# Kernel optimization log

Hardware: AMD Instinct MI355X
Metric: run time of the kernel (lower is better)

Reference implementation:

```python
import jax, jax.numpy as jnp
from jax import lax
import numpy as np


def setup_inputs() -> dict:
    key = jax.random.key(0)
    T, W = 2048, 30  # document length, max span width
    starts = jnp.repeat(jnp.arange(T, dtype=jnp.int32), W)      # [T*W]
    widths = jnp.tile(jnp.arange(W, dtype=jnp.int32), T)        # [T*W]
    ends = jnp.minimum(starts + widths, T - 1)
    spans = jnp.stack([starts, ends], axis=1)                   # [N,2], N=61440
    N = spans.shape[0]
    scores = jax.random.normal(key, (N,), dtype=jnp.float32)
    mask = jnp.ones((N,), dtype=jnp.float32)
    return {
        "spans": spans,
        "span_mention_scores": scores,
        "span_mask": mask,
        "token_num": T,
        "num_spans_to_keep": int(0.4 * T),
    }


def _greedy_non_crossing(spans, scores, mask, T, k):
    """Greedy NMS-style selection of up to k spans with no crossing overlap.
    Faithful to masked_topk_non_overlap: iterate candidates in descending
    (score + log(mask)) order; a candidate (s,e) is rejected iff it crosses
    an already-selected span, tracked via start_to_max_end / end_to_min_start
    tables. Sequential dependence expressed as lax.scan; the O(span_width)
    inner token loop is vectorized as an O(T) masked range query.
    """
    N = scores.shape[0]
    order = jnp.argsort(-(scores + jnp.log(mask)))  # descending sort
    starts = spans[:, 0].astype(jnp.int32)
    ends = spans[:, 1].astype(jnp.int32)
    tok = jnp.arange(T, dtype=jnp.int32)

    def step(carry, c):
        s2e, e2s, sel, cnt = carry
        s = starts[c]
        e = ends[c]
        # token_idx in (s, e] with start_to_max_end[token_idx] > e -> crossing
        cross1 = jnp.any((tok > s) & (tok <= e) & (s2e > e))
        # token_idx in [s, e) with 0 <= end_to_min_start[token_idx] < s -> crossing
        cross2 = jnp.any((tok >= s) & (tok < e) & (e2s >= 0) & (e2s < s))
        accept = jnp.logical_and(jnp.logical_not(cross1 | cross2), cnt < k)
        # start_to_max_end[s] = max(old, e) if accepted
        s2e = s2e.at[s].set(jnp.where(accept, jnp.maximum(s2e[s], e), s2e[s]))
        # end_to_min_start[e] = s if unset or s smaller, if accepted
        cur = e2s[e]
        e2s = e2s.at[e].set(jnp.where(accept & ((cur == -1) | (s < cur)), s, cur))
        sel = sel.at[c].set(sel[c] | accept)
        cnt = cnt + accept.astype(jnp.int32)
        return (s2e, e2s, sel, cnt), None

    init = (jnp.full((T,), -1, dtype=jnp.int32),
            jnp.full((T,), -1, dtype=jnp.int32),
            jnp.zeros((N,), dtype=bool),
            jnp.int32(0))
    (s2e, e2s, sel, cnt), _ = lax.scan(step, init, order)

    # sort selected candidates by (start, end); pad to fixed size k
    sort_key = jnp.where(sel, starts * T + ends, T * T)  # T*T > any valid key
    idx = jnp.argsort(sort_key)[:k]
    valid = jnp.arange(k) < cnt
    top_idx = jnp.where(valid, idx, 0)
    return top_idx, valid


def reference(spans, span_mention_scores, span_mask, token_num, num_spans_to_keep):
    top_idx, valid = _greedy_non_crossing(
        spans, span_mention_scores, span_mask, token_num, num_spans_to_keep)
    top_scores = jnp.where(valid, span_mention_scores[top_idx], 0.0)
    top_spans = jnp.where(valid[:, None], spans[top_idx], 0)
    return top_scores, top_idx, top_spans, valid
```

## Files before the change

kernel.cpp:

```cpp
#include <hip/hip_runtime.h>
#include <math.h>
#include <limits.h>

#define TPB   1024
#define TILE  1024
#define MAXT  2048
#define TPAD  64
#define MAXK  1024
#define MAXW  29
#define BATCH 1024
#define FLAGSTRIDE 16

struct SortSM {
  union {
    unsigned h[4 * 256];
    unsigned wcnt[16][256];
  };
  unsigned baseL[256];
  unsigned part[4][256];
};

__device__ inline void dbar(unsigned* flg, int nblk) {
  __syncthreads();
  if (threadIdx.x == 0) {
    __threadfence();
    atomicExch(&flg[blockIdx.x * FLAGSTRIDE], 1u);
  }
  if ((int)threadIdx.x < nblk) {
    int spin = 0;
    while (__hip_atomic_load(&flg[threadIdx.x * FLAGSTRIDE], __ATOMIC_ACQUIRE,
                             __HIP_MEMORY_SCOPE_AGENT) == 0u) {
      __builtin_amdgcn_s_sleep(2);
      if ((++spin & 255) == 0) {
        if (atomicAdd(&flg[threadIdx.x * FLAGSTRIDE], 0u) != 0u) break;
      }
    }
  }
  __syncthreads();
  if (threadIdx.x == 0) __threadfence();
  __syncthreads();
}

__global__ void __launch_bounds__(TPB, 4) sort_kernel(
    const float* __restrict__ scores, const float* __restrict__ mask,
    int N, int nT, unsigned* pflag, unsigned* ghist,
    unsigned* tileCnt, unsigned* keysA, unsigned* keysB, int* idxA, int* idxB) {
  __shared__ SortSM s;
  __shared__ unsigned base4[4][256];
  const int tid = threadIdx.x;
  const int lane = tid & 63;
  const int wave = tid >> 6;

  if (tid < 1024) s.h[tid] = 0;
  __syncthreads();
  {
    int i = blockIdx.x * TILE + tid;
    if (i < N) {
      float kf = scores[i] + logf(mask[i]);
      unsigned u = __float_as_uint(kf);
      u = (u & 0x80000000u) ? ~u : (u | 0x80000000u);
      u = ~u;
      keysA[i] = u;
      atomicAdd(&s.h[(u & 255u)], 1u);
      atomicAdd(&s.h[256 + ((u >> 8) & 255u)], 1u);
      atomicAdd(&s.h[512 + ((u >> 16) & 255u)], 1u);
      atomicAdd(&s.h[768 + (u >> 24)], 1u);
    }
    __syncthreads();
    if (tid < 1024 && s.h[tid]) atomicAdd(&ghist[tid], s.h[tid]);
  }
  dbar(pflag + (size_t)4 * nT * FLAGSTRIDE, nT);

  if (wave < 4) {
    const int p = wave;
    unsigned v0 = ghist[p * 256 + 4 * lane + 0];
    unsigned v1 = ghist[p * 256 + 4 * lane + 1];
    unsigned v2 = ghist[p * 256 + 4 * lane + 2];
    unsigned v3 = ghist[p * 256 + 4 * lane + 3];
    unsigned sum = v0 + v1 + v2 + v3;
    unsigned x = sum;
    for (int off = 1; off < 64; off <<= 1) {
      unsigned y = __shfl_up(x, off, 64);
      if (lane >= off) x += y;
    }
    unsigned excl = x - sum;
    base4[p][4 * lane + 0] = excl;
    base4[p][4 * lane + 1] = excl + v0;
    base4[p][4 * lane + 2] = excl + v0 + v1;
    base4[p][4 * lane + 3] = excl + v0 + v1 + v2;
  }
  __syncthreads();

  for (int p = 0; p < 4; ++p) {
    const unsigned* srck = (p & 1) ? keysB : keysA;
    const int*      srci = (p & 1) ? idxB : idxA;
    unsigned*       dstk = (p & 1) ? keysA : keysB;
    int*            dsti = (p & 1) ? idxA : idxB;
    const int shift = 8 * p;
    unsigned* flg = pflag + (size_t)p * nT * FLAGSTRIDE;

    for (int j = tid; j < 16 * 256; j += TPB)
      (&s.wcnt[0][0])[j] = 0;
    __syncthreads();

    int i = blockIdx.x * TILE + tid;
    bool v = (i < N);
    unsigned key = v ? srck[i] : 0u;
    int pay = v ? ((p == 0) ? i : srci[i]) : 0;
    unsigned d = (key >> shift) & 255u;
    unsigned long long mm = __ballot(v);
    #pragma unroll
    for (int b = 0; b < 8; ++b) {
      unsigned long long bb = __ballot((d >> b) & 1u);
      mm &= ((d >> b) & 1u) ? bb : ~bb;
    }
    unsigned rnk = (unsigned)__popcll(mm & ((1ull << lane) - 1ull));
    if (v && rnk == 0) s.wcnt[wave][d] = (unsigned)__popcll(mm);
    __syncthreads();
    if (tid < 256) {
      unsigned run = 0;
      #pragma unroll
      for (int g = 0; g < 16; ++g) {
        unsigned c = s.wcnt[g][tid];
        s.wcnt[g][tid] = run;
        run += c;
      }
      tileCnt[blockIdx.x * 256 + tid] = run;
    }
    __syncthreads();

    if (tid == 0) {
      __threadfence();
      atomicExch(&flg[blockIdx.x * FLAGSTRIDE], 1u);
    }
    if (tid < blockIdx.x) {
      while (atomicAdd(&flg[tid * FLAGSTRIDE], 0u) == 0u)
        __builtin_amdgcn_s_sleep(2);
    }
    __syncthreads();
    if (tid == 0) __threadfence();
    __syncthreads();

    {
      int digit = tid & 255;
      int chunk = tid >> 8;
      int b = blockIdx.x;
      int Q = (b + 3) >> 2;
      int t0 = chunk * Q;
      int t1 = t0 + Q; if (t1 > b) t1 = b;
      unsigned acc2 = 0;
      for (int t = t0; t < t1; ++t)
        acc2 += tileCnt[t * 256 + digit];
      s.part[chunk][digit] = acc2;
    }
    __syncthreads();
    if (tid < 256) {
      s.baseL[tid] = base4[p][tid] + s.part[0][tid] + s.part[1][tid]
                   + s.part[2][tid] + s.part[3][tid];
    }
    __syncthreads();
    if (v) {
      unsigned pos = s.baseL[d] + s.wcnt[wave][d] + rnk;
      dstk[pos] = key;
      dsti[pos] = pay;
    }
    if (p < 3) dbar(pflag + (size_t)(5 + p) * nT * FLAGSTRIDE, nT);
  }
}

__device__ inline bool precheck30(const unsigned* tabP, int cc, int cs, int ce) {
  if (cc < 0) return false;
  int w = ce - cs;
  bool crossed = false;
  #pragma unroll
  for (int off = 0; off <= MAXW; ++off) {
    unsigned tv = tabP[cs + off];
    crossed |= ((off >= 1) & (off <= w) & ((tv & 0xFFFFu) > (unsigned)(ce + 1)))
             | ((off < w) & ((tv >> 16) < (unsigned)cs));
  }
  for (int off = MAXW + 1; off <= w; ++off) {
    unsigned tv = tabP[cs + off];
    crossed |= ((tv & 0xFFFFu) > (unsigned)(ce + 1));
    if (off < w) crossed |= ((tv >> 16) < (unsigned)cs);
  }
  return !crossed;
}

__global__ void __launch_bounds__(TPB, 4) greedy_kernel(
    const int2* __restrict__ spans2, const int* __restrict__ spans,
    const float* __restrict__ scores, const int* __restrict__ order,
    const int* __restrict__ tnum_p, const int* __restrict__ keep_p,
    float* __restrict__ out, int N) {
  __shared__ unsigned tabP[MAXT + TPAD];
  __shared__ int2 tab[MAXT + TPAD];
  __shared__ unsigned long long acc[MAXK];
  __shared__ unsigned long long surv[BATCH];
  __shared__ unsigned long long Cmat[BATCH];
  __shared__ int wvs[16];
  __shared__ int gcnt;

  const int tid = threadIdx.x;
  const int lane = tid & 63;
  const int wave = tid >> 6;
  const int T  = tnum_p[0];
  const int k0 = keep_p[0];
  const int k  = (k0 < MAXK) ? k0 : MAXK;

  for (int t = tid; t < MAXT + TPAD; t += TPB) {
    tab[t] = make_int2(-1, INT_MAX);
    tabP[t] = 0xFFFF0000u;
  }
  if (tid == 0) gcnt = 0;
  __syncthreads();

  int cc = -1, cs = 0, ce = 0, nn = -1;
  if (tid < N)         cc = order[tid];
  if (BATCH + tid < N) nn = order[BATCH + tid];
  if (cc >= 0) { int2 sp = spans2[cc]; cs = sp.x; ce = sp.y; }

  int cnt = 0;
  for (int c0 = 0; c0 < N && cnt < k; c0 += BATCH) {
    int pc = nn, ps = 0, pe = 0;
    if (pc >= 0) { int2 sp = spans2[pc]; ps = sp.x; pe = sp.y; }
    int i2 = c0 + 2 * BATCH + tid;
    nn = (i2 < N) ? order[i2] : -1;

    bool ok = precheck30(tabP, cc, cs, ce);
    unsigned long long bal = __ballot(ok);
    if (lane == 0) wvs[wave] = (int)__popcll(bal);
    __syncthreads();
    int ns = 0, wb = 0;
    #pragma unroll
    for (int w2 = 0; w2 < 16; ++w2) {
      if (w2 == wave) wb = ns;
      ns += wvs[w2];
    }

    if (ns > 0) {
      if (ok) {
        int pos = wb + (int)__popcll(bal & ((1ull << lane) - 1ull));
        surv[pos] = ((unsigned long long)(unsigned)cs << 48)
                  | ((unsigned long long)(unsigned)ce << 32)
                  | (unsigned)cc;
      }
      __syncthreads();

      for (int v = tid; v < ns; v += TPB) {
        unsigned long long pk = surv[v];
        int gs = (int)(pk >> 48), ge = (int)((pk >> 32) & 0xFFFFu);
        int gbase = v & ~63;
        int m = ns - gbase; if (m > 64) m = 64;
        unsigned long long C = 0;
        for (int j = 0; j < m; ++j) {
          unsigned long long pj = surv[gbase + j];
          int sj = (int)(pj >> 48), ej = (int)((pj >> 32) & 0xFFFFu);
          bool cr = (gs < sj && sj <= ge && ej > ge) ||
                    (sj < gs && gs <= ej && ej < ge);
          C |= (unsigned long long)cr << j;
        }
        Cmat[v] = C;
      }
      __syncthreads();

      if (tid < 64) {
        bool dirty = false;
        for (int g = 0; g < ns && cnt < k; g += 64) {
          int m = ns - g; if (m > 64) m = 64;
          bool act = lane < m;
          int gs = 0, ge = 0, gc = 0;
          unsigned long long C = 0;
          if (act) {
            unsigned long long pk = surv[g + lane];
            gs = (int)(pk >> 48);
            ge = (int)((pk >> 32) & 0xFFFFu);
            gc = (int)(unsigned)pk;
            C  = Cmat[g + lane];
          }
          bool pre = act;
          if (dirty) {
            pre = act && precheck30(tabP, gc, gs, ge);
          }
          unsigned long long preB = __ballot(pre);
          if (preB == 0ull) continue;
          int np = (int)__popcll(preB);
          unsigned long long lower = (1ull << lane) - 1ull;
          unsigned long long accm;
          int cnt0g = cnt;
          if (np == 1) {
            accm = preB;
            cnt += 1;
          } else {
            unsigned long long Cl = C & lower;
            unsigned long long resolvedB = ~preB;
            accm = 0ull;
            while (true) {
              bool meUn   = ((resolvedB >> lane) & 1ull) == 0ull;
              bool killed = (Cl & accm) != 0ull;
              bool ready  = (Cl & ~resolvedB) == 0ull;
              unsigned long long newacc = __ballot(meUn && ready && !killed);
              unsigned long long newrej = __ballot(meUn && killed);
              if (!(newacc | newrej)) break;
              accm |= newacc;
              resolvedB |= (newacc | newrej);
            }
            int nacc = (int)__popcll(accm);
            if (cnt + nacc > k) {
              int room = k - cnt;
              bool a0 = ((accm >> lane) & 1ull) != 0ull;
              int ar = (int)__popcll(accm & lower);
              accm = __ballot(a0 && (ar < room));
              nacc = room;
            }
            cnt += nacc;
          }
          bool accme = ((accm >> lane) & 1ull) != 0ull;
          if (accme) {
            int rank = (int)__popcll(accm & lower);
            acc[cnt0g + rank] =
                ((unsigned long long)(unsigned)(gs * T + ge) << 32) | (unsigned)gc;
            atomicMax(&tab[gs].x, ge);
            atomicMin(&tab[ge].y, gs);
          }
          if (accme) {
            int2 tv = tab[gs];
            tabP[gs] = ((unsigned)(tv.y > 65535 ? 65535 : tv.y) << 16)
                     | (unsigned)(tv.x + 1);
            int2 tv2 = tab[ge];
            tabP[ge] = ((unsigned)(tv2.y > 65535 ? 65535 : tv2.y) << 16)
                     | (unsigned)(tv2.x + 1);
          }
          if (accm) dirty = true;
        }
        if (lane == 0) gcnt = cnt;
      }
      __syncthreads();
      cnt = gcnt;
    }

    cc = pc; cs = ps; ce = pe;
  }

  int M = 2;
  while (M < cnt) M <<= 1;
  for (int j = tid; j < M; j += TPB)
    if (j >= cnt) acc[j] = ~0ull;
  __syncthreads();
  for (int kk = 2; kk <= M; kk <<= 1) {
    for (int jj = kk >> 1; jj > 0; jj >>= 1) {
      for (int i3 = tid; i3 < M; i3 += TPB) {
        int ixj = i3 ^ jj;
        if (ixj > i3) {
          unsigned long long a = acc[i3], b = acc[ixj];
          bool up = ((i3 & kk) == 0);
          if ((a > b) == up) { acc[i3] = b; acc[ixj] = a; }
        }
      }
      __syncthreads();
    }
  }

  for (int j = tid; j < k0; j += TPB) {
    if (j < cnt) {
      int cand = (int)(acc[j] & 0xFFFFFFFFu);
      out[j]                  = scores[cand];
      out[k0 + j]             = (float)cand;
      out[2 * k0 + 2 * j]     = (float)spans[2 * cand];
      out[2 * k0 + 2 * j + 1] = (float)spans[2 * cand + 1];
      out[4 * k0 + j]         = 1.0f;
    } else {
      out[j]                  = 0.0f;
      out[k0 + j]             = 0.0f;
      out[2 * k0 + 2 * j]     = 0.0f;
      out[2 * k0 + 2 * j + 1] = 0.0f;
      out[4 * k0 + j]         = 0.0f;
    }
  }
}

extern "C" void kernel_launch(void* const* d_in, const int* in_sizes, int n_in,
                              void* d_out, int out_size, void* d_ws, size_t ws_size,
                              hipStream_t stream) {
  const int*   spans  = (const int*)d_in[0];
  const float* scores = (const float*)d_in[1];
  const float* mask   = (const float*)d_in[2];
  const int*   tnum   = (const int*)d_in[3];
  const int*   keep   = (const int*)d_in[4];
  const int N = in_sizes[1];
  const int nT = (N + TILE - 1) / TILE;

  unsigned* pflag   = (unsigned*)d_ws;
  unsigned* ghist   = pflag + (size_t)8 * nT * FLAGSTRIDE;
  unsigned* tileCnt = ghist + 1024;
  unsigned* keysA   = tileCnt + (size_t)nT * 256;
  unsigned* keysB   = keysA + N;
  int*      idxA    = (int*)(keysB + N);
  int*      idxB    = idxA + N;
  float*    out     = (float*)d_out;

  hipMemsetAsync(pflag, 0,
                 ((size_t)8 * nT * FLAGSTRIDE + 1024) * sizeof(unsigned),
                 stream);

  sort_kernel<<<nT, TPB, 0, stream>>>(scores, mask, N, nT, pflag, ghist,
                                      tileCnt, keysA, keysB, idxA, idxB);
  greedy_kernel<<<1, TPB, 0, stream>>>((const int2*)spans, spans, scores,
                                       idxA, tnum, keep, out, N);
}
```

Measured before the change: 227.6 us.

## Warp-specialize greedy loop: wave 0 resolves while other waves prefilter next batch

Splits the block into a resolver wave and 15 producer waves. The producers precheck candidates and build the crossing matrix for the next batch into double-buffered shared arrays, while wave 0 runs the sequential greedy acceptance on the previous batch. Producers coordinate through a spin-based LDS barrier, and the batch size drops to 960 to match the 15 producer waves. This aims to hide the serial resolve phase behind the parallel filter, but producers now precheck against a table that is one batch stale, so wave 0 must always rerun the precheck, and every iteration adds spin-wait overhead.

Result: faster. 219.6 us, median of 2 (-3.5%).

```diff
diff --git a/kernel.cpp b/kernel.cpp
--- a/kernel.cpp
+++ b/kernel.cpp
@@ -8,7 +8,7 @@
 #define TPAD  64
 #define MAXK  1024
 #define MAXW  29
-#define BATCH 1024
+#define BATCH 960
 #define FLAGSTRIDE 16
 
 struct SortSM {
@@ -186,6 +186,15 @@
   return !crossed;
 }
 
+__device__ inline void softbar(unsigned* sbar, unsigned target) {
+  if ((threadIdx.x & 63) == 0)
+    __hip_atomic_fetch_add(sbar, 1u, __ATOMIC_ACQ_REL,
+                           __HIP_MEMORY_SCOPE_WORKGROUP);
+  while (__hip_atomic_load(sbar, __ATOMIC_ACQUIRE,
+                           __HIP_MEMORY_SCOPE_WORKGROUP) < target)
+    __builtin_amdgcn_s_sleep(1);
+}
+
 __global__ void __launch_bounds__(TPB, 4) greedy_kernel(
     const int2* __restrict__ spans2, const int* __restrict__ spans,
     const float* __restrict__ scores, const int* __restrict__ order,
@@ -194,9 +203,11 @@
   __shared__ unsigned tabP[MAXT + TPAD];
   __shared__ int2 tab[MAXT + TPAD];
   __shared__ unsigned long long acc[MAXK];
-  __shared__ unsigned long long surv[BATCH];
-  __shared__ unsigned long long Cmat[BATCH];
+  __shared__ unsigned long long surv0[BATCH], surv1[BATCH];
+  __shared__ unsigned long long cmat0[BATCH], cmat1[BATCH];
   __shared__ int wvs[16];
+  __shared__ int ns_s[2];
+  __shared__ unsigned sbar;
   __shared__ int gcnt;
 
   const int tid = threadIdx.x;
@@ -210,134 +221,137 @@
     tab[t] = make_int2(-1, INT_MAX);
     tabP[t] = 0xFFFF0000u;
   }
-  if (tid == 0) gcnt = 0;
+  if (tid == 0) { gcnt = 0; ns_s[0] = 0; ns_s[1] = 0; sbar = 0u; }
+  if (tid < 16) wvs[tid] = 0;
   __syncthreads();
 
   int cc = -1, cs = 0, ce = 0, nn = -1;
-  if (tid < N)         cc = order[tid];
-  if (BATCH + tid < N) nn = order[BATCH + tid];
-  if (cc >= 0) { int2 sp = spans2[cc]; cs = sp.x; ce = sp.y; }
-
+  if (tid >= 64) {
+    int q = tid - 64;
+    if (q < N)          cc = order[q];
+    if (BATCH + q < N)  nn = order[BATCH + q];
+    if (cc >= 0) { int2 sp = spans2[cc]; cs = sp.x; ce = sp.y; }
+  }
+
+  unsigned long long* sA = surv0; unsigned long long* cA = cmat0;
+  unsigned long long* sB = surv1; unsigned long long* cB = cmat1;
+  int bufA = 0;
   int cnt = 0;
-  for (int c0 = 0; c0 < N && cnt < k; c0 += BATCH) {
-    int pc = nn, ps = 0, pe = 0;
-    if (pc >= 0) { int2 sp = spans2[pc]; ps = sp.x; pe = sp.y; }
-    int i2 = c0 + 2 * BATCH + tid;
-    nn = (i2 < N) ? order[i2] : -1;
-
-    bool ok = precheck30(tabP, cc, cs, ce);
-    unsigned long long bal = __ballot(ok);
-    if (lane == 0) wvs[wave] = (int)__popcll(bal);
-    __syncthreads();
-    int ns = 0, wb = 0;
-    #pragma unroll
-    for (int w2 = 0; w2 < 16; ++w2) {
-      if (w2 == wave) wb = ns;
-      ns += wvs[w2];
-    }
-
-    if (ns > 0) {
+  int it = 0;
+  for (long c0 = 0; c0 < (long)N + BATCH && cnt < k; c0 += BATCH, ++it) {
+    if (wave == 0) {
+      int nsA = ns_s[bufA];
+      for (int g = 0; g < nsA && cnt < k; g += 64) {
+        int m = nsA - g; if (m > 64) m = 64;
+        bool act = lane < m;
+        int gs = 0, ge = 0, gc = 0;
+        unsigned long long C = 0;
+        if (act) {
+          unsigned long long pk = sA[g + lane];
+          gs = (int)(pk >> 48);
+          ge = (int)((pk >> 32) & 0xFFFFu);
+          gc = (int)(unsigned)pk;
+          C  = cA[g + lane];
+        }
+        bool pre = act && precheck30(tabP, gc, gs, ge);
+        unsigned long long preB = __ballot(pre);
+        if (preB == 0ull) continue;
+        int np = (int)__popcll(preB);
+        unsigned long long lower = (1ull << lane) - 1ull;
+        unsigned long long accm;
+        int cnt0g = cnt;
+        if (np == 1) {
+          accm = preB;
+          cnt += 1;
+        } else {
+          unsigned long long Cl = C & lower;
+          unsigned long long resolvedB = ~preB;
+          accm = 0ull;
+          while (true) {
+            bool meUn   = ((resolvedB >> lane) & 1ull) == 0ull;
+            bool killed = (Cl & accm) != 0ull;
+            bool ready  = (Cl & ~resolvedB) == 0ull;
+            unsigned long long newacc = __ballot(meUn && ready && !killed);
+            unsigned long long newrej = __ballot(meUn && killed);
+            if (!(newacc | newrej)) break;
+            accm |= newacc;
+            resolvedB |= (newacc | newrej);
+          }
+          int nacc = (int)__popcll(accm);
+          if (cnt + nacc > k) {
+            int room = k - cnt;
+            bool a0 = ((accm >> lane) & 1ull) != 0ull;
+            int ar = (int)__popcll(accm & lower);
+            accm = __ballot(a0 && (ar < room));
+            nacc = room;
+          }
+          cnt += nacc;
+        }
+        bool accme = ((accm >> lane) & 1ull) != 0ull;
+        if (accme) {
+          int rank = (int)__popcll(accm & lower);
+          acc[cnt0g + rank] =
+              ((unsigned long long)(unsigned)(gs * T + ge) << 32) | (unsigned)gc;
+          atomicMax(&tab[gs].x, ge);
+          atomicMin(&tab[ge].y, gs);
+        }
+        if (accme) {
+          int2 tv = tab[gs];
+          tabP[gs] = ((unsigned)(tv.y > 65535 ? 65535 : tv.y) << 16)
+                   | (unsigned)(tv.x + 1);
+          int2 tv2 = tab[ge];
+          tabP[ge] = ((unsigned)(tv2.y > 65535 ? 65535 : tv2.y) << 16)
+                   | (unsigned)(tv2.x + 1);
+        }
+      }
+      if (lane == 0) gcnt = cnt;
+    } else {
+      int q = tid - 64;
+      int pc = nn, ps = 0, pe = 0;
+      if (pc >= 0) { int2 sp = spans2[pc]; ps = sp.x; pe = sp.y; }
+      long i2 = c0 + 2 * (long)BATCH + q;
+      nn = (i2 < N) ? order[i2] : -1;
+
+      bool ok = precheck30(tabP, cc, cs, ce);
+      unsigned long long bal = __ballot(ok);
+      if (lane == 0) wvs[wave] = (int)__popcll(bal);
+      softbar(&sbar, 15u * (2u * (unsigned)it + 1u));
+      int ns = 0, wb = 0;
+      #pragma unroll
+      for (int w2 = 1; w2 < 16; ++w2) {
+        if (w2 == wave) wb = ns;
+        ns += wvs[w2];
+      }
       if (ok) {
         int pos = wb + (int)__popcll(bal & ((1ull << lane) - 1ull));
-        surv[pos] = ((unsigned long long)(unsigned)cs << 48)
-                  | ((unsigned long long)(unsigned)ce << 32)
-                  | (unsigned)cc;
-      }
-      __syncthreads();
-
-      for (int v = tid; v < ns; v += TPB) {
-        unsigned long long pk = surv[v];
+        sB[pos] = ((unsigned long long)(unsigned)cs << 48)
+                | ((unsigned long long)(unsigned)ce << 32)
+                | (unsigned)cc;
+      }
+      if (wave == 1 && lane == 0) ns_s[bufA ^ 1] = ns;
+      softbar(&sbar, 15u * (2u * (unsigned)it + 2u));
+      for (int v = q; v < ns; v += BATCH) {
+        unsigned long long pk = sB[v];
         int gs = (int)(pk >> 48), ge = (int)((pk >> 32) & 0xFFFFu);
         int gbase = v & ~63;
         int m = ns - gbase; if (m > 64) m = 64;
         unsigned long long C = 0;
         for (int j = 0; j < m; ++j) {
-          unsigned long long pj = surv[gbase + j];
+          unsigned long long pj = sB[gbase + j];
           int sj = (int)(pj >> 48), ej = (int)((pj >> 32) & 0xFFFFu);
           bool cr = (gs < sj && sj <= ge && ej > ge) ||
                     (sj < gs && gs <= ej && ej < ge);
           C |= (unsigned long long)cr << j;
         }
-        Cmat[v] = C;
-      }
-      __syncthreads();
-
-      if (tid < 64) {
-        bool dirty = false;
-        for (int g = 0; g < ns && cnt < k; g += 64) {
-          int m = ns - g; if (m > 64) m = 64;
-          bool act = lane < m;
-          int gs = 0, ge = 0, gc = 0;
-          unsigned long long C = 0;
-          if (act) {
-            unsigned long long pk = surv[g + lane];
-            gs = (int)(pk >> 48);
-            ge = (int)((pk >> 32) & 0xFFFFu);
-            gc = (int)(unsigned)pk;
-            C  = Cmat[g + lane];
-          }
-          bool pre = act;
-          if (dirty) {
-            pre = act && precheck30(tabP, gc, gs, ge);
-          }
-          unsigned long long preB = __ballot(pre);
-          if (preB == 0ull) continue;
-          int np = (int)__popcll(preB);
-          unsigned long long lower = (1ull << lane) - 1ull;
-          unsigned long long accm;
-          int cnt0g = cnt;
-          if (np == 1) {
-            accm = preB;
-            cnt += 1;
-          } else {
-            unsigned long long Cl = C & lower;
-            unsigned long long resolvedB = ~preB;
-            accm = 0ull;
-            while (true) {
-              bool meUn   = ((resolvedB >> lane) & 1ull) == 0ull;
-              bool killed = (Cl & accm) != 0ull;
-              bool ready  = (Cl & ~resolvedB) == 0ull;
-              unsigned long long newacc = __ballot(meUn && ready && !killed);
-              unsigned long long newrej = __ballot(meUn && killed);
-              if (!(newacc | newrej)) break;
-              accm |= newacc;
-              resolvedB |= (newacc | newrej);
-            }
-            int nacc = (int)__popcll(accm);
-            if (cnt + nacc > k) {
-              int room = k - cnt;
-              bool a0 = ((accm >> lane) & 1ull) != 0ull;
-              int ar = (int)__popcll(accm & lower);
-              accm = __ballot(a0 && (ar < room));
-              nacc = room;
-            }
-            cnt += nacc;
-          }
-          bool accme = ((accm >> lane) & 1ull) != 0ull;
-          if (accme) {
-            int rank = (int)__popcll(accm & lower);
-            acc[cnt0g + rank] =
-                ((unsigned long long)(unsigned)(gs * T + ge) << 32) | (unsigned)gc;
-            atomicMax(&tab[gs].x, ge);
-            atomicMin(&tab[ge].y, gs);
-          }
-          if (accme) {
-            int2 tv = tab[gs];
-            tabP[gs] = ((unsigned)(tv.y > 65535 ? 65535 : tv.y) << 16)
-                     | (unsigned)(tv.x + 1);
-            int2 tv2 = tab[ge];
-            tabP[ge] = ((unsigned)(tv2.y > 65535 ? 65535 : tv2.y) << 16)
-                     | (unsigned)(tv2.x + 1);
-          }
-          if (accm) dirty = true;
-        }
-        if (lane == 0) gcnt = cnt;
-      }
-      __syncthreads();
-      cnt = gcnt;
-    }
-
-    cc = pc; cs = ps; ce = pe;
+        cB[v] = C;
+      }
+      cc = pc; cs = ps; ce = pe;
+    }
+    __syncthreads();
+    cnt = gcnt;
+    { unsigned long long* t = sA; sA = sB; sB = t;
+      t = cA; cA = cB; cB = t; }
+    bufA ^= 1;
   }
 
   int M = 2;
```
